# Kernel tuning notes

Hardware: AMD Instinct MI355X
Metric: run time of the kernel (lower is better)

Reference implementation:

```python
import jax, jax.numpy as jnp
import numpy as np

N_NODES = 50000
N_EDGES = 640000
IN_DIM = 128
HID = 128
OUT_DIM = 16
BATCH = 2
EPS = 1e-5


def setup_inputs() -> dict:
    key = jax.random.key(0)
    ks = jax.random.split(key, 12)
    x = jax.random.normal(ks[0], (BATCH, N_NODES, IN_DIM), dtype=jnp.float32)
    edge_index = jax.random.randint(ks[1], (2, N_EDGES), 0, N_NODES, dtype=jnp.int32)
    # learned per-edge log-weights (initialized ~0 like nn.Parameter(zeros), small noise for a nontrivial test)
    edge_weight_param = 0.01 * jax.random.normal(ks[2], (N_EDGES,), dtype=jnp.float32)
    s1 = 1.0 / np.sqrt(IN_DIM)
    s2 = 1.0 / np.sqrt(HID)
    W1 = jax.random.uniform(ks[3], (IN_DIM, HID), minval=-s1, maxval=s1, dtype=jnp.float32)
    b1 = jnp.zeros((HID,), jnp.float32)
    W2 = jax.random.uniform(ks[4], (HID, HID), minval=-s2, maxval=s2, dtype=jnp.float32)
    b2 = jnp.zeros((HID,), jnp.float32)
    g1 = jnp.ones((HID,), jnp.float32); be1 = jnp.zeros((HID,), jnp.float32)
    g2 = jnp.ones((HID,), jnp.float32); be2 = jnp.zeros((HID,), jnp.float32)
    Wc = jax.random.uniform(ks[5], (HID, OUT_DIM), minval=-s2, maxval=s2, dtype=jnp.float32)
    bc = jax.random.uniform(ks[6], (OUT_DIM,), minval=-s2, maxval=s2, dtype=jnp.float32)
    return {"x": x, "edge_index": edge_index, "edge_weight_param": edge_weight_param,
            "W1": W1, "b1": b1, "W2": W2, "b2": b2,
            "g1": g1, "be1": be1, "g2": g2, "be2": be2,
            "Wc": Wc, "bc": bc}


def _gcn_norm(edge_index, edge_weight):
    # PyG GCNConv: add self-loops (weight 1), symmetric D^-1/2 A D^-1/2 normalization
    row = jnp.concatenate([edge_index[0], jnp.arange(N_NODES, dtype=edge_index.dtype)])
    col = jnp.concatenate([edge_index[1], jnp.arange(N_NODES, dtype=edge_index.dtype)])
    ew = jnp.concatenate([edge_weight, jnp.ones((N_NODES,), edge_weight.dtype)])
    deg = jax.ops.segment_sum(ew, col, num_segments=N_NODES)
    dinv = jnp.where(deg > 0, jax.lax.rsqrt(jnp.maximum(deg, 1e-30)), 0.0)
    norm = dinv[row] * ew * dinv[col]
    return row, col, norm


def _gcn_conv(x, W, b, row, col, norm):
    # x: [B, N, F_in] -> [B, N, F_out]; gather-scale-scatter over edges
    xw = x @ W                                   # [B, N, H]
    msg = xw[:, row, :] * norm[None, :, None]    # [B, E+N, H]
    out = jax.vmap(lambda m: jax.ops.segment_sum(m, col, num_segments=N_NODES))(msg)
    return out + b


def _batchnorm(h, gamma, beta):
    # training-mode BN over flattened (B*N) rows, biased variance, eps=1e-5
    B, N, F = h.shape
    hf = h.reshape(-1, F)
    mu = hf.mean(axis=0)
    var = hf.var(axis=0)
    return (((hf - mu) * jax.lax.rsqrt(var + EPS)) * gamma + beta).reshape(B, N, F)


def reference(x, edge_index, edge_weight_param, W1, b1, W2, b2, g1, be1, g2, be2, Wc, bc):
    edge_weight = jnp.exp(edge_weight_param)  # learned exp edge weights
    row, col, norm = _gcn_norm(edge_index, edge_weight)
    h = jax.nn.relu(_gcn_conv(x, W1, b1, row, col, norm))
    h = _batchnorm(h, g1, be1)
    # dropout is identity in eval / deterministic reference
    h = jax.nn.relu(_gcn_conv(h, W2, b2, row, col, norm))
    h = _batchnorm(h, g2, be2)
    return h @ Wc + bc  # [B, N, OUT_DIM]
```

## Files before the change

kernel.cpp:

```cpp
#include <hip/hip_runtime.h>
#include <hip/hip_bf16.h>
#include <cstdint>
#include <cstddef>

#define N_NODES 50000
#define N_EDGES 640000
#define ROWS    100000
#define HID     128
#define OUTD    16
#define AGG_BLOCKS 2048
#define MID_BLOCKS 32
#define SCAN_BLOCKS 196
#define GEMM_BLOCKS 512
#define GEMM_TILES  (ROWS / 16)
#define EG_BLOCKS   3500
#define EG_GEMM_WAVES 4000

typedef __attribute__((ext_vector_type(8))) uint16_t ushort8;
typedef __attribute__((ext_vector_type(8))) __bf16   bf16x8;
typedef __attribute__((ext_vector_type(4))) float    floatx4;

union FragU { ushort8 u; bf16x8 b; };

__device__ __forceinline__ float bf_lo(uint32_t u){
  union { uint32_t u; float f; } c; c.u = u << 16; return c.f;
}
__device__ __forceinline__ float bf_hi(uint32_t u){
  union { uint32_t u; float f; } c; c.u = u & 0xffff0000u; return c.f;
}
__device__ __forceinline__ uint16_t f2bf(float f){
  union { float f; uint32_t u; } c; c.f = f;
  uint32_t u = c.u;
  uint32_t r = (u + 0x7fffu + ((u >> 16) & 1u)) >> 16;
  return (uint16_t)r;
}

__device__ __forceinline__ void pack_w(int t, const float* __restrict__ W,
                                       const float* sca ,
                                       uint16_t* __restrict__ WP){
  int L = t & 63;
  int s = (t >> 6) & 3;
  int c = t >> 8;
  int n = (c >> 1) * 32 + 2 * (L & 15) + (c & 1);
  int k0 = s * 32 + (L >> 4) * 8;
  ushort8 r;
#pragma unroll
  for (int j = 0; j < 8; j++){
    float w = W[(size_t)(k0 + j) * HID + n];
    if (sca) w *= sca[k0 + j];
    r[j] = f2bf(w);
  }
  *((ushort8*)(WP + (size_t)t * 8)) = r;
}

__global__ void k_initpack(unsigned long long* __restrict__ dc,
                           const float* __restrict__ W1, uint16_t* __restrict__ WP1){
  int b = blockIdx.x;
  if (b < SCAN_BLOCKS){
    int i = b * 256 + threadIdx.x;
    if (i < N_NODES) dc[i] = 0ull;
  } else {
    pack_w((b - SCAN_BLOCKS) * 256 + threadIdx.x, W1, nullptr, WP1);
  }
}

__global__ __launch_bounds__(256, 2) void k_edge_gemm1(const int* __restrict__ ei,
                                                       const float* __restrict__ ewp,
                                                       unsigned long long* __restrict__ dc,
                                                       unsigned int* __restrict__ slot,
                                                       const float* __restrict__ X,
                                                       const uint16_t* __restrict__ WP,
                                                       uint16_t* __restrict__ Y){
  const int b = blockIdx.x;
  const int g = b % 7;
  if (g < 5){
    const int eb = (b / 7) * 5 + g;
    const int e = eb * 256 + threadIdx.x;
    float w = expf(ewp[e]);
    int c = ei[N_EDGES + e];
    unsigned long long inc = (1ull << 44) | (unsigned long long)(w * 1048576.0f + 0.5f);
    unsigned long long old = atomicAdd(&dc[c], inc);
    slot[e] = (unsigned int)(old >> 44);
    return;
  }
  const int lane = threadIdx.x & 63;
  const int wid  = threadIdx.x >> 6;
  const int gw   = ((b / 7) * 2 + (g - 5)) * 4 + wid;
  const int m    = lane & 15;
  const int kq   = lane >> 4;

  FragU wf[8][4];
#pragma unroll
  for (int c = 0; c < 8; c++)
#pragma unroll
    for (int s = 0; s < 4; s++)
      wf[c][s].u = *((const ushort8*)(WP + (size_t)(((c * 4 + s) * 64 + lane) * 8)));

  uint32_t* Yu = (uint32_t*)Y;
  for (int t = gw; t < GEMM_TILES; t += EG_GEMM_WAVES){
    const int row0 = t * 16;
    FragU af[4];
#pragma unroll
    for (int s = 0; s < 4; s++){
      const float* p = X + (size_t)(row0 + m) * HID + s * 32 + kq * 8;
      floatx4 f0 = *((const floatx4*)p);
      floatx4 f1 = *((const floatx4*)(p + 4));
      ushort8 r;
#pragma unroll
      for (int j = 0; j < 4; j++){ r[j] = f2bf(f0[j]); r[j + 4] = f2bf(f1[j]); }
      af[s].u = r;
    }
    floatx4 acc[8];
#pragma unroll
    for (int c = 0; c < 8; c++) acc[c] = floatx4{0.f, 0.f, 0.f, 0.f};
#pragma unroll
    for (int s = 0; s < 4; s++)
#pragma unroll
      for (int c = 0; c < 8; c++)
        acc[c] = __builtin_amdgcn_mfma_f32_16x16x32_bf16(af[s].b, wf[c][s].b, acc[c], 0, 0, 0);
#pragma unroll
    for (int t4 = 0; t4 < 4; t4++)
#pragma unroll
      for (int i = 0; i < 4; i++){
        uint32_t pr = (uint32_t)f2bf(acc[2 * t4][i]) | ((uint32_t)f2bf(acc[2 * t4 + 1][i]) << 16);
        Yu[(size_t)(row0 + kq * 4 + i) * 64 + t4 * 16 + m] = pr;
      }
  }
}

__global__ void k_scan_bsum(const unsigned long long* __restrict__ dc, int* __restrict__ bsum,
                            float* __restrict__ dinv){
  __shared__ int sd[256];
  int tid = threadIdx.x;
  int i = blockIdx.x * 256 + tid;
  int cnt = 0;
  if (i < N_NODES){
    unsigned long long v = dc[i];
    cnt = (int)(v >> 44);
    float deg = 1.0f + (float)((double)(v & ((1ull << 44) - 1)) * (1.0 / 1048576.0));
    dinv[i] = 1.0f / sqrtf(deg);
  }
  sd[tid] = cnt;
  __syncthreads();
  for (int off = 128; off > 0; off >>= 1){
    if (tid < off) sd[tid] += sd[tid + off];
    __syncthreads();
  }
  if (tid == 0) bsum[blockIdx.x] = sd[0];
}

__global__ void k_scan_write(const unsigned long long* __restrict__ dc, const int* __restrict__ bsum,
                             int* __restrict__ rp){
  __shared__ int sb[256];
  __shared__ int sd[256];
  int tid = threadIdx.x;
  sb[tid] = (tid < SCAN_BLOCKS && tid < blockIdx.x) ? bsum[tid] : 0;
  __syncthreads();
  for (int off = 128; off > 0; off >>= 1){
    if (tid < off) sb[tid] += sb[tid + off];
    __syncthreads();
  }
  const int base = sb[0];

  int i = blockIdx.x * 256 + tid;
  int v = (i < N_NODES) ? (int)(dc[i] >> 44) : 0;
  sd[tid] = v;
  __syncthreads();
  for (int off = 1; off < 256; off <<= 1){
    int t = (tid >= off) ? sd[tid - off] : 0;
    __syncthreads();
    sd[tid] += t;
    __syncthreads();
  }
  if (i < N_NODES) rp[i] = base + sd[tid] - v;
  if (blockIdx.x == 0 && tid == 0) rp[N_NODES] = N_EDGES;
}

__global__ void k_fill(const int* __restrict__ ei, const float* __restrict__ ewp,
                       const float* __restrict__ dinv, const unsigned int* __restrict__ slot,
                       const int* __restrict__ rp, unsigned long long* __restrict__ edg){
  int e = blockIdx.x * 256 + threadIdx.x;
  if (e < N_EDGES){
    int r = ei[e];
    int c = ei[N_EDGES + e];
    float w = expf(ewp[e]);
    float nrm = dinv[r] * w * dinv[c];
    int p = rp[c] + (int)slot[e];
    edg[p] = ((unsigned long long)__float_as_uint(nrm) << 32) | (unsigned int)r;
  }
}

__global__ __launch_bounds__(256, 2) void k_gemm2(const uint16_t* __restrict__ X,
                                                  const uint16_t* __restrict__ WP,
                                                  uint16_t* __restrict__ Y){
  const int lane = threadIdx.x & 63;
  const int wid  = threadIdx.x >> 6;
  const int gw   = blockIdx.x * 4 + wid;
  const int nw   = GEMM_BLOCKS * 4;
  const int m    = lane & 15;
  const int kq   = lane >> 4;

  FragU wf[8][4];
#pragma unroll
  for (int c = 0; c < 8; c++)
#pragma unroll
    for (int s = 0; s < 4; s++)
      wf[c][s].u = *((const ushort8*)(WP + (size_t)(((c * 4 + s) * 64 + lane) * 8)));

  uint32_t* Yu = (uint32_t*)Y;
  for (int t = gw; t < GEMM_TILES; t += nw){
    const int row0 = t * 16;
    FragU af[4];
#pragma unroll
    for (int s = 0; s < 4; s++)
      af[s].u = *((const ushort8*)(X + (size_t)(row0 + m) * HID + s * 32 + kq * 8));
    floatx4 acc[8];
#pragma unroll
    for (int c = 0; c < 8; c++) acc[c] = floatx4{0.f, 0.f, 0.f, 0.f};
#pragma unroll
    for (int s = 0; s < 4; s++)
#pragma unroll
      for (int c = 0; c < 8; c++)
        acc[c] = __builtin_amdgcn_mfma_f32_16x16x32_bf16(af[s].b, wf[c][s].b, acc[c], 0, 0, 0);
#pragma unroll
    for (int t4 = 0; t4 < 4; t4++)
#pragma unroll
      for (int i = 0; i < 4; i++){
        uint32_t pr = (uint32_t)f2bf(acc[2 * t4][i]) | ((uint32_t)f2bf(acc[2 * t4 + 1][i]) << 16);
        Yu[(size_t)(row0 + kq * 4 + i) * 64 + t4 * 16 + m] = pr;
      }
  }
}

__global__ __launch_bounds__(256) void k_cls_mfma(const uint16_t* __restrict__ H,
                                                  const uint16_t* __restrict__ WPC,
                                                  const float* __restrict__ cvec,
                                                  float* __restrict__ out){
  const int lane = threadIdx.x & 63;
  const int wid  = threadIdx.x >> 6;
  const int gw   = blockIdx.x * 4 + wid;
  const int nw   = GEMM_BLOCKS * 4;
  const int m    = lane & 15;
  const int kq   = lane >> 4;

  FragU wf[4];
#pragma unroll
  for (int s = 0; s < 4; s++)
    wf[s].u = *((const ushort8*)(WPC + (size_t)((s * 64 + lane) * 8)));
  const float cv = cvec[m];

  for (int t = gw; t < GEMM_TILES; t += nw){
    const int row0 = t * 16;
    FragU af[4];
#pragma unroll
    for (int s = 0; s < 4; s++)
      af[s].u = *((const ushort8*)(H + (size_t)(row0 + m) * HID + s * 32 + kq * 8));
    floatx4 acc = floatx4{0.f, 0.f, 0.f, 0.f};
#pragma unroll
    for (int s = 0; s < 4; s++)
      acc = __builtin_amdgcn_mfma_f32_16x16x32_bf16(af[s].b, wf[s].b, acc, 0, 0, 0);
#pragma unroll
    for (int i = 0; i < 4; i++)
      out[(size_t)(row0 + kq * 4 + i) * OUTD + m] = acc[i] + cv;
  }
}

__global__ __launch_bounds__(256) void k_agg(const uint16_t* __restrict__ XW,
                                             const int* __restrict__ rp,
                                             const unsigned long long* __restrict__ edg,
                                             const float* __restrict__ dinv,
                                             const float* __restrict__ bias,
                                             const float* __restrict__ cvec,
                                             uint16_t* __restrict__ H,
                                             float* __restrict__ psum,
                                             float* __restrict__ pssq){
  __shared__ float lsum[128];
  __shared__ float lssq[128];
  const int tid = threadIdx.x;
  if (tid < 128){ lsum[tid] = 0.f; lssq[tid] = 0.f; }
  __syncthreads();

  const int lane = tid & 63;
  const int wid  = tid >> 6;
  const int gw   = blockIdx.x * 4 + wid;
  const int nw   = AGG_BLOCKS * 4;
  const uint32_t* Xu = (const uint32_t*)XW;
  uint32_t* Hu = (uint32_t*)H;
  const int f0 = lane * 2;
  const float b0 = bias[f0], b1 = bias[f0 + 1];
  const float c0 = cvec ? cvec[f0] : 0.f;
  const float c1 = cvec ? cvec[f0 + 1] : 0.f;
  float ts0 = 0.f, ts1 = 0.f, tq0 = 0.f, tq1 = 0.f;

  int node = gw;
  if (node < N_NODES){
    int e0 = rp[node], e1 = rp[node + 1];
    float di = dinv[node];
    uint32_t s0 = Xu[(size_t)node * 64 + lane];
    uint32_t s1 = Xu[(size_t)(N_NODES + node) * 64 + lane];
    while (true){
      const int nn = node + nw;
      const bool more = (nn < N_NODES);
      int ne0 = 0, ne1 = 0; float ndi = 0.f; uint32_t ns0 = 0, ns1 = 0;
      if (more){
        ne0 = rp[nn]; ne1 = rp[nn + 1];
        ndi = dinv[nn];
        ns0 = Xu[(size_t)nn * 64 + lane];
        ns1 = Xu[(size_t)(N_NODES + nn) * 64 + lane];
      }

      const float sn = di * di;
      float a0x = sn * bf_lo(s0), a0y = sn * bf_hi(s0);
      float a1x = sn * bf_lo(s1), a1y = sn * bf_hi(s1);
      float wsum = sn;
      int e = e0;
      for (; e + 8 <= e1; e += 8){
        unsigned long long myrec = edg[e + (lane & 7)];
        uint32_t rlo = (uint32_t)myrec;
        uint32_t rhi = (uint32_t)(myrec >> 32);
        int srcs[8]; float ws[8];
#pragma unroll
        for (int u = 0; u < 8; u++){
          srcs[u] = __builtin_amdgcn_readlane(rlo, u);
          ws[u] = __uint_as_float((uint32_t)__builtin_amdgcn_readlane((int)rhi, u));
        }
        uint32_t q0[8], q1[8];
#pragma unroll
        for (int u = 0; u < 8; u++){
          q0[u] = Xu[(size_t)(uint32_t)srcs[u] * 64 + lane];
          q1[u] = Xu[(size_t)(N_NODES + (uint32_t)srcs[u]) * 64 + lane];
        }
#pragma unroll
        for (int u = 0; u < 8; u++){
          a0x = fmaf(ws[u], bf_lo(q0[u]), a0x); a0y = fmaf(ws[u], bf_hi(q0[u]), a0y);
          a1x = fmaf(ws[u], bf_lo(q1[u]), a1x); a1y = fmaf(ws[u], bf_hi(q1[u]), a1y);
          wsum += ws[u];
        }
      }
      for (; e + 4 <= e1; e += 4){
        unsigned long long myrec = edg[e + (lane & 3)];
        uint32_t rlo = (uint32_t)myrec;
        uint32_t rhi = (uint32_t)(myrec >> 32);
        int srcs[4]; float ws[4];
#pragma unroll
        for (int u = 0; u < 4; u++){
          srcs[u] = __builtin_amdgcn_readlane(rlo, u);
          ws[u] = __uint_as_float((uint32_t)__builtin_amdgcn_readlane((int)rhi, u));
        }
        uint32_t q0[4], q1[4];
#pragma unroll
        for (int u = 0; u < 4; u++){
          q0[u] = Xu[(size_t)(uint32_t)srcs[u] * 64 + lane];
          q1[u] = Xu[(size_t)(N_NODES + (uint32_t)srcs[u]) * 64 + lane];
        }
#pragma unroll
        for (int u = 0; u < 4; u++){
          a0x = fmaf(ws[u], bf_lo(q0[u]), a0x); a0y = fmaf(ws[u], bf_hi(q0[u]), a0y);
          a1x = fmaf(ws[u], bf_lo(q1[u]), a1x); a1y = fmaf(ws[u], bf_hi(q1[u]), a1y);
          wsum += ws[u];
        }
      }
      for (; e < e1; e++){
        unsigned long long rec = edg[e];
        size_t src = (uint32_t)rec;
        float w = __uint_as_float((uint32_t)(rec >> 32));
        uint32_t g0 = Xu[src * 64 + lane];
        uint32_t g1 = Xu[(N_NODES + src) * 64 + lane];
        a0x = fmaf(w, bf_lo(g0), a0x); a0y = fmaf(w, bf_hi(g0), a0y);
        a1x = fmaf(w, bf_lo(g1), a1x); a1y = fmaf(w, bf_hi(g1), a1y);
        wsum += w;
      }
      a0x = fmaxf(fmaf(wsum, c0, a0x) + b0, 0.f); a0y = fmaxf(fmaf(wsum, c1, a0y) + b1, 0.f);
      a1x = fmaxf(fmaf(wsum, c0, a1x) + b0, 0.f); a1y = fmaxf(fmaf(wsum, c1, a1y) + b1, 0.f);
      Hu[(size_t)node * 64 + lane]             = (uint32_t)f2bf(a0x) | ((uint32_t)f2bf(a0y) << 16);
      Hu[(size_t)(N_NODES + node) * 64 + lane] = (uint32_t)f2bf(a1x) | ((uint32_t)f2bf(a1y) << 16);
      ts0 += a0x + a1x; ts1 += a0y + a1y;
      tq0 += a0x * a0x + a1x * a1x; tq1 += a0y * a0y + a1y * a1y;

      if (!more) break;
      node = nn; e0 = ne0; e1 = ne1; di = ndi; s0 = ns0; s1 = ns1;
    }
  }

  atomicAdd(&lsum[f0],     ts0); atomicAdd(&lsum[f0 + 1], ts1);
  atomicAdd(&lssq[f0],     tq0); atomicAdd(&lssq[f0 + 1], tq1);
  __syncthreads();
  if (tid < 128){
    psum[(size_t)blockIdx.x * 128 + tid] = lsum[tid];
    pssq[(size_t)blockIdx.x * 128 + tid] = lssq[tid];
  }
}

__global__ __launch_bounds__(256) void k_bnmid(const float* __restrict__ psum,
                                               const float* __restrict__ pssq,
                                               float* __restrict__ msum,
                                               float* __restrict__ mssq){
  __shared__ float ss[2][128];
  __shared__ float sq[2][128];
  const int tid = threadIdx.x;
  const int f  = tid & 127;
  const int sl = tid >> 7;
  const int rows_per = AGG_BLOCKS / MID_BLOCKS;
  const int base = blockIdx.x * rows_per;
  float s = 0.f, q = 0.f;
  for (int r = base + sl; r < base + rows_per; r += 2){
    s += psum[(size_t)r * 128 + f];
    q += pssq[(size_t)r * 128 + f];
  }
  ss[sl][f] = s; sq[sl][f] = q;
  __syncthreads();
  if (tid < 128){
    msum[(size_t)blockIdx.x * 128 + tid] = ss[0][tid] + ss[1][tid];
    mssq[(size_t)blockIdx.x * 128 + tid] = sq[0][tid] + sq[1][tid];
  }
}

__device__ __forceinline__ void bn_finalize_lds(const float* __restrict__ msum,
                                                const float* __restrict__ mssq,
                                                const float* __restrict__ gamma,
                                                const float* __restrict__ beta,
                                                float* ssc, float* ssh){
  const int tid = threadIdx.x;
  if (tid < 128){
    float S = 0.f, Q = 0.f;
#pragma unroll
    for (int b = 0; b < MID_BLOCKS; b++){
      S += msum[(size_t)b * 128 + tid];
      Q += mssq[(size_t)b * 128 + tid];
    }
    const float inv = 1.0f / (float)ROWS;
    float mu = S * inv;
    float var = fmaxf(Q * inv - mu * mu, 0.f);
    float rstd = 1.0f / sqrtf(var + 1e-5f);
    float sc = gamma[tid] * rstd;
    ssc[tid] = sc;
    ssh[tid] = fmaf(-mu, sc, beta[tid]);
  }
  __syncthreads();
}

__global__ void k_prep2(const float* __restrict__ msum, const float* __restrict__ mssq,
                        const float* __restrict__ gamma, const float* __restrict__ beta,
                        const float* __restrict__ W2,
                        uint16_t* __restrict__ WP2, float* __restrict__ C2){
  __shared__ float ssc[128];
  __shared__ float ssh[128];
  bn_finalize_lds(msum, mssq, gamma, beta, ssc, ssh);
  if (blockIdx.x < 8){
    pack_w(blockIdx.x * 256 + threadIdx.x, W2, ssc, WP2);
  } else if (threadIdx.x < 128){
    const int j = threadIdx.x;
    float a = 0.f;
    for (int k = 0; k < HID; k++) a = fmaf(ssh[k], W2[(size_t)k * HID + j], a);
    C2[j] = a;
  }
}

__global__ void k_prepc(const float* __restrict__ msum, const float* __restrict__ mssq,
                        const float* __restrict__ gamma, const float* __restrict__ beta,
                        const float* __restrict__ Wc, const float* __restrict__ bc,
                        uint16_t* __restrict__ WPC, float* __restrict__ CVC){
  __shared__ float ssc[128];
  __shared__ float ssh[128];
  bn_finalize_lds(msum, mssq, gamma, beta, ssc, ssh);
  if (blockIdx.x == 0){
    int t = threadIdx.x;
    int L = t & 63;
    int s = t >> 6;
    int n = L & 15;
    int k0 = s * 32 + (L >> 4) * 8;
    ushort8 r;
#pragma unroll
    for (int j = 0; j < 8; j++)
      r[j] = f2bf(ssc[k0 + j] * Wc[(size_t)(k0 + j) * OUTD + n]);
    *((ushort8*)(WPC + (size_t)t * 8)) = r;
  } else if (threadIdx.x < OUTD){
    const int j = threadIdx.x;
    float a = bc[j];
    for (int k = 0; k < HID; k++) a = fmaf(ssh[k], Wc[(size_t)k * OUTD + j], a);
    CVC[j] = a;
  }
}

extern "C" void kernel_launch(void* const* d_in, const int* in_sizes, int n_in,
                              void* d_out, int out_size, void* d_ws, size_t ws_size,
                              hipStream_t stream){
  const float* x   = (const float*)d_in[0];
  const int*   ei  = (const int*)d_in[1];
  const float* ewp = (const float*)d_in[2];
  const float* W1  = (const float*)d_in[3];
  const float* b1  = (const float*)d_in[4];
  const float* W2  = (const float*)d_in[5];
  const float* b2  = (const float*)d_in[6];
  const float* g1  = (const float*)d_in[7];
  const float* be1 = (const float*)d_in[8];
  const float* g2  = (const float*)d_in[9];
  const float* be2 = (const float*)d_in[10];
  const float* Wc  = (const float*)d_in[11];
  const float* bc  = (const float*)d_in[12];
  float* out = (float*)d_out;

  char* wsb = (char*)d_ws;
  size_t off = 0;
  auto give = [&](size_t bytes) -> void* {
    void* p = wsb + off;
    off = (off + bytes + 255) & ~(size_t)255;
    return p;
  };
  uint16_t* XW  = (uint16_t*)give((size_t)ROWS * 128 * 2);
  uint16_t* Hb  = (uint16_t*)give((size_t)ROWS * 128 * 2);
  unsigned long long* DC  = (unsigned long long*)give((size_t)N_NODES * 8);
  unsigned long long* EDG = (unsigned long long*)give((size_t)N_EDGES * 8);
  unsigned int* SLOT = (unsigned int*)give((size_t)N_EDGES * 4);
  float* DINV   = (float*)give((size_t)N_NODES * 4);
  int*   RP     = (int*)give((size_t)(N_NODES + 1) * 4);
  int*   BSUM   = (int*)give(1024);
  float* PSUM   = (float*)give((size_t)AGG_BLOCKS * 128 * 4);
  float* PSSQ   = (float*)give((size_t)AGG_BLOCKS * 128 * 4);
  float* MSUM   = (float*)give((size_t)MID_BLOCKS * 128 * 4);
  float* MSSQ   = (float*)give((size_t)MID_BLOCKS * 128 * 4);
  uint16_t* WP1 = (uint16_t*)give((size_t)HID * HID * 2);
  uint16_t* WP2 = (uint16_t*)give((size_t)HID * HID * 2);
  uint16_t* WPC = (uint16_t*)give((size_t)HID * OUTD * 2);
  float* C2     = (float*)give(512);
  float* CVC    = (float*)give(64);
  (void)ws_size; (void)n_in; (void)in_sizes; (void)out_size;

  k_initpack<<<SCAN_BLOCKS + 8, 256, 0, stream>>>(DC, W1, WP1);
  k_edge_gemm1<<<EG_BLOCKS, 256, 0, stream>>>(ei, ewp, DC, SLOT, x, WP1, XW);
  k_scan_bsum<<<SCAN_BLOCKS, 256, 0, stream>>>(DC, BSUM, DINV);
  k_scan_write<<<SCAN_BLOCKS, 256, 0, stream>>>(DC, BSUM, RP);
  k_fill<<<(N_EDGES + 255) / 256, 256, 0, stream>>>(ei, ewp, DINV, SLOT, RP, EDG);
  k_agg<<<AGG_BLOCKS, 256, 0, stream>>>(XW, RP, EDG, DINV, b1, nullptr, Hb, PSUM, PSSQ);
  k_bnmid<<<MID_BLOCKS, 256, 0, stream>>>(PSUM, PSSQ, MSUM, MSSQ);
  k_prep2<<<9, 256, 0, stream>>>(MSUM, MSSQ, g1, be1, W2, WP2, C2);
  k_gemm2<<<GEMM_BLOCKS, 256, 0, stream>>>(Hb, WP2, XW);
  k_agg<<<AGG_BLOCKS, 256, 0, stream>>>(XW, RP, EDG, DINV, b2, C2, Hb, PSUM, PSSQ);
  k_bnmid<<<MID_BLOCKS, 256, 0, stream>>>(PSUM, PSSQ, MSUM, MSSQ);
  k_prepc<<<2, 256, 0, stream>>>(MSUM, MSSQ, g2, be2, Wc, bc, WPC, CVC);
  k_cls_mfma<<<GEMM_BLOCKS, 256, 0, stream>>>(Hb, WPC, CVC, out);
}
```

Before: 316.1 us.

## Merge edge-count and GEMM1 work per block, mask agg tail, widen gemm2 grid

The fused edge/GEMM1 kernel previously split blocks into edge-counting and GEMM roles. Now every block does 256 edge atomics and then one 16-row GEMM tile per wave, with 2500 blocks covering both the edges and the tiles exactly. The aggregation tail replaces the 4-wide loop and scalar loop with a single masked 8-wide batch, cutting loop overhead and serial dependent loads for low-degree nodes at the cost of some wasted gathers. The gemm2 grid is doubled to 1024 blocks.

```diff
diff --git a/kernel.cpp b/kernel.cpp
--- a/kernel.cpp
+++ b/kernel.cpp
@@ -12,9 +12,10 @@
 #define MID_BLOCKS 32
 #define SCAN_BLOCKS 196
 #define GEMM_BLOCKS 512
+#define GEMM2_BLOCKS 1024
 #define GEMM_TILES  (ROWS / 16)
-#define EG_BLOCKS   3500
-#define EG_GEMM_WAVES 4000
+#define EG_BLOCKS   2500
+#define EG_WAVES    (EG_BLOCKS * 4)
 
 typedef __attribute__((ext_vector_type(8))) uint16_t ushort8;
 typedef __attribute__((ext_vector_type(8))) __bf16   bf16x8;
@@ -71,21 +72,18 @@
                                                        const float* __restrict__ X,
                                                        const uint16_t* __restrict__ WP,
                                                        uint16_t* __restrict__ Y){
-  const int b = blockIdx.x;
-  const int g = b % 7;
-  if (g < 5){
-    const int eb = (b / 7) * 5 + g;
-    const int e = eb * 256 + threadIdx.x;
+  {
+    const int e = blockIdx.x * 256 + threadIdx.x;
     float w = expf(ewp[e]);
     int c = ei[N_EDGES + e];
     unsigned long long inc = (1ull << 44) | (unsigned long long)(w * 1048576.0f + 0.5f);
     unsigned long long old = atomicAdd(&dc[c], inc);
     slot[e] = (unsigned int)(old >> 44);
-    return;
   }
   const int lane = threadIdx.x & 63;
   const int wid  = threadIdx.x >> 6;
-  const int gw   = ((b / 7) * 2 + (g - 5)) * 4 + wid;
+  const int gw   = blockIdx.x * 4 + wid;
+  if (gw >= GEMM_TILES) return;
   const int m    = lane & 15;
   const int kq   = lane >> 4;
 
@@ -97,35 +95,33 @@
       wf[c][s].u = *((const ushort8*)(WP + (size_t)(((c * 4 + s) * 64 + lane) * 8)));
 
   uint32_t* Yu = (uint32_t*)Y;
-  for (int t = gw; t < GEMM_TILES; t += EG_GEMM_WAVES){
-    const int row0 = t * 16;
-    FragU af[4];
-#pragma unroll
-    for (int s = 0; s < 4; s++){
-      const float* p = X + (size_t)(row0 + m) * HID + s * 32 + kq * 8;
-      floatx4 f0 = *((const floatx4*)p);
-      floatx4 f1 = *((const floatx4*)(p + 4));
-      ushort8 r;
-#pragma unroll
-      for (int j = 0; j < 4; j++){ r[j] = f2bf(f0[j]); r[j + 4] = f2bf(f1[j]); }
-      af[s].u = r;
+  const int row0 = gw * 16;
+  FragU af[4];
+#pragma unroll
+  for (int s = 0; s < 4; s++){
+    const float* p = X + (size_t)(row0 + m) * HID + s * 32 + kq * 8;
+    floatx4 f0 = *((const floatx4*)p);
+    floatx4 f1 = *((const floatx4*)(p + 4));
+    ushort8 r;
+#pragma unroll
+    for (int j = 0; j < 4; j++){ r[j] = f2bf(f0[j]); r[j + 4] = f2bf(f1[j]); }
+    af[s].u = r;
+  }
+  floatx4 acc[8];
+#pragma unroll
+  for (int c = 0; c < 8; c++) acc[c] = floatx4{0.f, 0.f, 0.f, 0.f};
+#pragma unroll
+  for (int s = 0; s < 4; s++)
+#pragma unroll
+    for (int c = 0; c < 8; c++)
+      acc[c] = __builtin_amdgcn_mfma_f32_16x16x32_bf16(af[s].b, wf[c][s].b, acc[c], 0, 0, 0);
+#pragma unroll
+  for (int t4 = 0; t4 < 4; t4++)
+#pragma unroll
+    for (int i = 0; i < 4; i++){
+      uint32_t pr = (uint32_t)f2bf(acc[2 * t4][i]) | ((uint32_t)f2bf(acc[2 * t4 + 1][i]) << 16);
+      Yu[(size_t)(row0 + kq * 4 + i) * 64 + t4 * 16 + m] = pr;
     }
-    floatx4 acc[8];
-#pragma unroll
-    for (int c = 0; c < 8; c++) acc[c] = floatx4{0.f, 0.f, 0.f, 0.f};
-#pragma unroll
-    for (int s = 0; s < 4; s++)
-#pragma unroll
-      for (int c = 0; c < 8; c++)
-        acc[c] = __builtin_amdgcn_mfma_f32_16x16x32_bf16(af[s].b, wf[c][s].b, acc[c], 0, 0, 0);
-#pragma unroll
-    for (int t4 = 0; t4 < 4; t4++)
-#pragma unroll
-      for (int i = 0; i < 4; i++){
-        uint32_t pr = (uint32_t)f2bf(acc[2 * t4][i]) | ((uint32_t)f2bf(acc[2 * t4 + 1][i]) << 16);
-        Yu[(size_t)(row0 + kq * 4 + i) * 64 + t4 * 16 + m] = pr;
-      }
-  }
 }
 
 __global__ void k_scan_bsum(const unsigned long long* __restrict__ dc, int* __restrict__ bsum,
@@ -196,7 +192,7 @@
   const int lane = threadIdx.x & 63;
   const int wid  = threadIdx.x >> 6;
   const int gw   = blockIdx.x * 4 + wid;
-  const int nw   = GEMM_BLOCKS * 4;
+  const int nw   = GEMM2_BLOCKS * 4;
   const int m    = lane & 15;
   const int kq   = lane >> 4;
 
@@ -337,38 +333,31 @@
           wsum += ws[u];
         }
       }
-      for (; e + 4 <= e1; e += 4){
-        unsigned long long myrec = edg[e + (lane & 3)];
+      if (e < e1){
+        const int rem = e1 - e;
+        const int myu = lane & 7;
+        unsigned long long myrec = edg[e + (myu < rem ? myu : 0)];
         uint32_t rlo = (uint32_t)myrec;
         uint32_t rhi = (uint32_t)(myrec >> 32);
-        int srcs[4]; float ws[4];
-#pragma unroll
-        for (int u = 0; u < 4; u++){
+        int srcs[8]; float ws[8];
+#pragma unroll
+        for (int u = 0; u < 8; u++){
           srcs[u] = __builtin_amdgcn_readlane(rlo, u);
-          ws[u] = __uint_as_float((uint32_t)__builtin_amdgcn_readlane((int)rhi, u));
+          float w = __uint_as_float((uint32_t)__builtin_amdgcn_readlane((int)rhi, u));
+          ws[u] = (u < rem) ? w : 0.f;
         }
-        uint32_t q0[4], q1[4];
-#pragma unroll
-        for (int u = 0; u < 4; u++){
+        uint32_t q0[8], q1[8];
+#pragma unroll
+        for (int u = 0; u < 8; u++){
           q0[u] = Xu[(size_t)(uint32_t)srcs[u] * 64 + lane];
           q1[u] = Xu[(size_t)(N_NODES + (uint32_t)srcs[u]) * 64 + lane];
         }
 #pragma unroll
-        for (int u = 0; u < 4; u++){
+        for (int u = 0; u < 8; u++){
           a0x = fmaf(ws[u], bf_lo(q0[u]), a0x); a0y = fmaf(ws[u], bf_hi(q0[u]), a0y);
           a1x = fmaf(ws[u], bf_lo(q1[u]), a1x); a1y = fmaf(ws[u], bf_hi(q1[u]), a1y);
           wsum += ws[u];
         }
-      }
-      for (; e < e1; e++){
-        unsigned long long rec = edg[e];
-        size_t src = (uint32_t)rec;
-        float w = __uint_as_float((uint32_t)(rec >> 32));
-        uint32_t g0 = Xu[src * 64 + lane];
-        uint32_t g1 = Xu[(N_NODES + src) * 64 + lane];
-        a0x = fmaf(w, bf_lo(g0), a0x); a0y = fmaf(w, bf_hi(g0), a0y);
-        a1x = fmaf(w, bf_lo(g1), a1x); a1y = fmaf(w, bf_hi(g1), a1y);
-        wsum += w;
       }
       a0x = fmaxf(fmaf(wsum, c0, a0x) + b0, 0.f); a0y = fmaxf(fmaf(wsum, c1, a0y) + b1, 0.f);
       a1x = fmaxf(fmaf(wsum, c0, a1x) + b0, 0.f); a1y = fmaxf(fmaf(wsum, c1, a1y) + b1, 0.f);
@@ -534,7 +523,7 @@
   k_agg<<<AGG_BLOCKS, 256, 0, stream>>>(XW, RP, EDG, DINV, b1, nullptr, Hb, PSUM, PSSQ);
   k_bnmid<<<MID_BLOCKS, 256, 0, stream>>>(PSUM, PSSQ, MSUM, MSSQ);
   k_prep2<<<9, 256, 0, stream>>>(MSUM, MSSQ, g1, be1, W2, WP2, C2);
-  k_gemm2<<<GEMM_BLOCKS, 256, 0, stream>>>(Hb, WP2, XW);
+  k_gemm2<<<GEMM2_BLOCKS, 256, 0, stream>>>(Hb, WP2, XW);
   k_agg<<<AGG_BLOCKS, 256, 0, stream>>>(XW, RP, EDG, DINV, b2, C2, Hb, PSUM, PSSQ);
   k_bnmid<<<MID_BLOCKS, 256, 0, stream>>>(PSUM, PSSQ, MSUM, MSSQ);
   k_prepc<<<2, 256, 0, stream>>>(MSUM, MSSQ, g2, be2, Wc, bc, WPC, CVC);
```

Result: slower. 337.9 us (+6.9%).
